# Performance work log

Measured on AMD Instinct MI355X. Metric: run time of the kernel, lower is better.

Reference implementation:

```python
import jax, jax.numpy as jnp
import numpy as np

K = 8            # NEAREST_K
IN = 68          # input_size = 64 + 4
EO = 32          # edge_output_size
FEAT = IN * 2 + EO * 4  # 264
EMB = 32         # linear_embedding
NCLS = 2
N = 768
EPS = 1e-5


def lrelu(x):
    return jnp.where(x >= 0, x, 0.01 * x)


def setup_inputs() -> dict:
    key = jax.random.key(0)
    ks = jax.random.split(key, 16)

    def w(k, fan_in, fan_out):
        return jax.random.normal(k, (fan_in, fan_out), jnp.float32) / np.float32(np.sqrt(fan_in))

    return {
        "feat0": jax.random.normal(ks[0], (N, IN), jnp.float32),
        "feat1": jax.random.normal(ks[1], (N, IN), jnp.float32),
        # edge_conv1: Linear(IN*K, EO) -> LeakyReLU -> Linear(EO, EO) -> LeakyReLU
        "ec1_w1": w(ks[2], IN * K, EO), "ec1_b1": jnp.zeros((EO,), jnp.float32),
        "ec1_w2": w(ks[3], EO, EO),     "ec1_b2": jnp.zeros((EO,), jnp.float32),
        # edge_conv2: Linear(EO*K, EO) -> LeakyReLU -> Linear(EO, EO) -> LeakyReLU
        "ec2_w1": w(ks[4], EO * K, EO), "ec2_b1": jnp.zeros((EO,), jnp.float32),
        "ec2_w2": w(ks[5], EO, EO),     "ec2_b2": jnp.zeros((EO,), jnp.float32),
        # linear head: BN(FEAT) -> Linear(FEAT,EMB) -> LReLU -> Linear(EMB,EMB) -> LReLU -> Linear(EMB,NCLS)
        "bn_g": jnp.ones((FEAT,), jnp.float32), "bn_b": jnp.zeros((FEAT,), jnp.float32),
        "lin1_w": w(ks[6], FEAT, EMB), "lin1_b": jnp.zeros((EMB,), jnp.float32),
        "lin2_w": w(ks[7], EMB, EMB),  "lin2_b": jnp.zeros((EMB,), jnp.float32),
        "lin3_w": w(ks[8], EMB, NCLS), "lin3_b": jnp.zeros((NCLS,), jnp.float32),
    }


def _pairs_for_graph(feat, ec1_w1, ec1_b1, ec1_w2, ec1_b2,
                     ec2_w1, ec2_b1, ec2_w2, ec2_b2):
    n = feat.shape[0]
    # kNN on first 4 dims via pairwise L1 distance (includes self, dist 0)
    coords = feat[:, :4]
    dist = jnp.abs(coords[:, None, :] - coords[None, :, :]).sum(-1)  # [n, n]
    _, idx = jax.lax.top_k(-dist, K)  # [n, K] smallest distances

    # EdgeConv 1: gather neighbor features, flatten feature-major (matches torch transpose+view)
    e1 = feat[idx]                                  # [n, K, IN]
    e1 = jnp.swapaxes(e1, 1, 2).reshape(n, IN * K)  # [n, IN*K]
    e1 = lrelu(lrelu(e1 @ ec1_w1 + ec1_b1) @ ec1_w2 + ec1_b2)  # [n, EO]

    # EdgeConv 2 on edge1 outputs
    e2 = e1[idx]                                    # [n, K, EO]
    e2 = jnp.swapaxes(e2, 1, 2).reshape(n, EO * K)  # [n, EO*K]
    e2 = lrelu(lrelu(e2 @ ec2_w1 + ec2_b1) @ ec2_w2 + ec2_b2)  # [n, EO]

    x = jnp.concatenate([feat, e1, e2], axis=-1)    # [n, IN + 2*EO] = [n, 132]
    # upper-triangle (i<j) all-pairs concat, row-major order == torch masked_select of triu mask
    iu, ju = jnp.triu_indices(n, k=1)
    return jnp.concatenate([x[iu], x[ju]], axis=-1)  # [n(n-1)/2, FEAT]


def reference(feat0, feat1, ec1_w1, ec1_b1, ec1_w2, ec1_b2,
              ec2_w1, ec2_b1, ec2_w2, ec2_b2,
              bn_g, bn_b, lin1_w, lin1_b, lin2_w, lin2_b, lin3_w, lin3_b):
    ec = (ec1_w1, ec1_b1, ec1_w2, ec1_b2, ec2_w1, ec2_b1, ec2_w2, ec2_b2)
    x = jnp.concatenate([_pairs_for_graph(feat0, *ec),
                         _pairs_for_graph(feat1, *ec)], axis=0)  # [P, FEAT]
    # BatchNorm1d in training mode: batch statistics (biased variance)
    mu = x.mean(axis=0)
    var = x.var(axis=0)
    x = (x - mu) * jax.lax.rsqrt(var + EPS) * bn_g + bn_b
    x = lrelu(x @ lin1_w + lin1_b)
    x = lrelu(x @ lin2_w + lin2_b)
    return x @ lin3_w + lin3_b  # [P, NCLS]
```

## Files before the change

### kernel.cpp

```cpp
#include <hip/hip_runtime.h>

#define NN 768
#define IN_F 68
#define KNN 8
#define EO 32
#define FEAT 264
#define HALF_FEAT 132
#define EMB 32
#define NPAIR 294528

typedef __attribute__((ext_vector_type(8))) short bf16x8;
typedef __attribute__((ext_vector_type(4))) float f32x4;

static __device__ __forceinline__ int pack_chop2(float x0, float x1) {
  return __builtin_amdgcn_perm(__float_as_uint(x1), __float_as_uint(x0), 0x07060302);
}
static __device__ __forceinline__ float chop(float x) {
  return __uint_as_float(__float_as_uint(x) & 0xffff0000u);
}


__global__ void __launch_bounds__(128) topk_ec1_kernel(
    const float* __restrict__ feat0, const float* __restrict__ feat1,
    const float* __restrict__ w1, const float* __restrict__ b1,
    const float* __restrict__ w2, const float* __restrict__ b2,
    int* __restrict__ idx_out, float* __restrict__ e1out)
{
  const int i = blockIdx.x, g = blockIdx.y;
  const float* __restrict__ feat = g ? feat1 : feat0;
  const int tid = threadIdx.x;
  const int lane = tid & 63, wv = tid >> 6;

  __shared__ unsigned long long keys[128*8];
  __shared__ int nbr[8];
  __shared__ float gl[KNN*IN_F];
  __shared__ float hsh[EO];
  __shared__ float part1[2][EO];
  __shared__ float part2[4][EO];

  const float4 ci = *(const float4*)(feat + i*IN_F);

  float4 cand[6];
#pragma unroll
  for (int t = 0; t < 6; t++)
    cand[t] = *(const float4*)(feat + (tid + 128*t)*IN_F);

  float bd[8]; int bidx[8];
#pragma unroll
  for (int k = 0; k < 8; k++) { bd[k] = 1e30f; bidx[k] = 0; }
#pragma unroll
  for (int t = 0; t < 6; t++) {
    const int j = tid + 128*t;
    float d = fabsf(ci.x - cand[t].x);
    d += fabsf(ci.y - cand[t].y);
    d += fabsf(ci.z - cand[t].z);
    d += fabsf(ci.w - cand[t].w);
    if (d < bd[7]) {
#pragma unroll
      for (int k = 7; k >= 1; k--) {
        if (d < bd[k-1])    { bd[k] = bd[k-1]; bidx[k] = bidx[k-1]; }
        else if (d < bd[k]) { bd[k] = d;       bidx[k] = j; }
      }
      if (d < bd[0]) { bd[0] = d; bidx[0] = j; }
    }
  }
#pragma unroll
  for (int k = 0; k < 8; k++)
    keys[tid*8+k] = ((unsigned long long)__float_as_uint(bd[k]) << 32) | (unsigned)bidx[k];
  __syncthreads();

  if (wv == 0) {
    int posA = 0, posB = 0;
#pragma unroll
    for (int r = 0; r < 8; r++) {
      unsigned long long ha = keys[lane*8 + posA];
      unsigned long long hb = keys[(lane+64)*8 + posB];
      unsigned long long mn = ha < hb ? ha : hb;
#pragma unroll
      for (int s = 32; s >= 1; s >>= 1) {
        unsigned long long o = __shfl_xor(mn, s, 64);
        mn = (o < mn) ? o : mn;
      }
      if (ha == mn) posA++;
      else if (hb == mn) posB++;
      if (lane == 0) {
        int nb = (int)(mn & 0xffffffffull);
        nbr[r] = nb;
        idx_out[(g*NN+i)*8 + r] = nb;
      }
    }
  }
  __syncthreads();

  for (int z = tid; z < KNN*17; z += 128) {
    int k = z / 17, q = z - k*17;
    *(float4*)&gl[k*IN_F + q*4] = *(const float4*)(feat + nbr[k]*IN_F + q*4);
  }
  __syncthreads();

  const int e = lane & 31, hf = lane >> 5;
  float ak[4];
#pragma unroll
  for (int k = 0; k < 4; k++) ak[k] = 0.f;
  const int cbeg = hf*34;
  const int kbase = wv*4;
  for (int c = cbeg; c < cbeg+34; c++) {
#pragma unroll
    for (int k = 0; k < 4; k++)
      ak[k] += gl[(kbase+k)*IN_F+c] * w1[(c*8+kbase+k)*EO + e];
  }
  float acc = (ak[0]+ak[1])+(ak[2]+ak[3]);
  acc += __shfl_xor(acc, 32, 64);
  if (hf == 0) part1[wv][e] = acc;
  __syncthreads();
  if (tid < 32) {
    float h = part1[0][tid] + part1[1][tid] + b1[tid];
    hsh[tid] = fmaxf(h, 0.01f*h);
  }
  __syncthreads();

  const int qq = tid >> 5, ee = tid & 31;
  {
    float o0=0.f, o1=0.f, o2=0.f, o3=0.f;
    const int mbeg = qq*8;
#pragma unroll
    for (int m = mbeg; m < mbeg+8; m += 4) {
      o0 += hsh[m+0] * w2[(m+0)*EO + ee];
      o1 += hsh[m+1] * w2[(m+1)*EO + ee];
      o2 += hsh[m+2] * w2[(m+2)*EO + ee];
      o3 += hsh[m+3] * w2[(m+3)*EO + ee];
    }
    part2[qq][ee] = ((o0+o1)+(o2+o3));
  }
  __syncthreads();
  if (tid < 32) {
    float o = b2[tid] + ((part2[0][tid]+part2[1][tid])+(part2[2][tid]+part2[3][tid]));
    o = fmaxf(o, 0.01f*o);
    e1out[(g*NN+i)*EO + tid] = o;
  }
}

__global__ void __launch_bounds__(64) ec2_kernel(
    const int* __restrict__ idx, const float* __restrict__ e1,
    const float* __restrict__ w1, const float* __restrict__ b1,
    const float* __restrict__ w2, const float* __restrict__ b2,
    float* __restrict__ e2out)
{
  const int i = blockIdx.x, g = blockIdx.y;
  const int lane = threadIdx.x;
  __shared__ float gl[KNN*EO];
  __shared__ float hsh[EO];
  {
    const int k = lane >> 3, q = lane & 7;
    const int nb = idx[(g*NN+i)*8 + k];
    *(float4*)&gl[k*EO + q*4] = *(const float4*)(e1 + (g*NN+nb)*EO + q*4);
  }
  __syncthreads();
  const int e = lane & 31, hf = lane >> 5;
  float ak[8];
#pragma unroll
  for (int k = 0; k < 8; k++) ak[k] = 0.f;
  const int cbeg = hf*16;
  for (int c = cbeg; c < cbeg+16; c++) {
#pragma unroll
    for (int k = 0; k < 8; k++)
      ak[k] += gl[k*EO+c] * w1[(c*8+k)*EO + e];
  }
  float acc = ((ak[0]+ak[1])+(ak[2]+ak[3])) + ((ak[4]+ak[5])+(ak[6]+ak[7]));
  acc += __shfl_xor(acc, 32, 64);
  if (hf == 0) {
    float h = acc + b1[e];
    hsh[e] = fmaxf(h, 0.01f*h);
  }
  __syncthreads();
  if (lane < 32) {
    float o0=0.f, o1=0.f, o2=0.f, o3=0.f;
#pragma unroll
    for (int m = 0; m < 32; m += 4) {
      o0 += hsh[m+0] * w2[(m+0)*EO + lane];
      o1 += hsh[m+1] * w2[(m+1)*EO + lane];
      o2 += hsh[m+2] * w2[(m+2)*EO + lane];
      o3 += hsh[m+3] * w2[(m+3)*EO + lane];
    }
    float o = b2[lane] + ((o0+o1)+(o2+o3));
    o = fmaxf(o, 0.01f*o);
    e2out[(g*NN+i)*EO + lane] = o;
  }
}

__global__ void __launch_bounds__(256) stats_kernel(
    const float* __restrict__ feat0, const float* __restrict__ feat1,
    const float* __restrict__ e1, const float* __restrict__ e2,
    const float* __restrict__ bn_g,
    float* __restrict__ mu_out, float* __restrict__ sg_out)
{
  const int c = blockIdx.x;
  const int tid = threadIdx.x;
  double s1=0, s2=0, q1=0, q2=0;
  for (int t = tid; t < 2*NN; t += 256) {
    int g = t >= NN;
    int i = t - g*NN;
    float val;
    if (c < IN_F)      val = (g ? feat1 : feat0)[i*IN_F + c];
    else if (c < 100)  val = e1[(g*NN+i)*EO + (c-IN_F)];
    else               val = e2[(g*NN+i)*EO + (c-100)];
    double dv = val;
    double wf = (double)(NN-1-i), wsnd = (double)i;
    s1 += wf*dv;  s2 += wsnd*dv;
    double dq = dv*dv;
    q1 += wf*dq;  q2 += wsnd*dq;
  }
#pragma unroll
  for (int off = 32; off >= 1; off >>= 1) {
    s1 += __shfl_xor(s1, off, 64);
    s2 += __shfl_xor(s2, off, 64);
    q1 += __shfl_xor(q1, off, 64);
    q2 += __shfl_xor(q2, off, 64);
  }
  __shared__ double red[4][4];
  const int w = tid >> 6;
  if ((tid & 63) == 0) { red[w][0]=s1; red[w][1]=s2; red[w][2]=q1; red[w][3]=q2; }
  __syncthreads();
  if (tid == 0) {
    double t0 = red[0][0]+red[1][0]+red[2][0]+red[3][0];
    double t1 = red[0][1]+red[1][1]+red[2][1]+red[3][1];
    double t2 = red[0][2]+red[1][2]+red[2][2]+red[3][2];
    double t3 = red[0][3]+red[1][3]+red[2][3]+red[3][3];
    const double M2 = 2.0 * (double)NPAIR;
    double mu1 = t0/M2, mu2 = t1/M2;
    double v1 = t2/M2 - mu1*mu1;
    double v2 = t3/M2 - mu2*mu2;
    mu_out[c]           = (float)mu1;
    mu_out[HALF_FEAT+c] = (float)mu2;
    sg_out[c]           = (float)((double)bn_g[c] / sqrt(v1 + 1e-5));
    sg_out[HALF_FEAT+c] = (float)((double)bn_g[HALF_FEAT+c] / sqrt(v2 + 1e-5));
  }
}

__global__ void __launch_bounds__(64) uv_c0_kernel(
    const float* __restrict__ feat0, const float* __restrict__ feat1,
    const float* __restrict__ e1, const float* __restrict__ e2,
    const float* __restrict__ sg, const float* __restrict__ mu,
    const float* __restrict__ bn_b,
    const float* __restrict__ lin1_w, const float* __restrict__ lin1_b,
    float* __restrict__ u, float* __restrict__ v, float* __restrict__ c0g)
{
  const int i = blockIdx.x, g = blockIdx.y;
  const int t = threadIdx.x;
  if (i == NN) {
    if (g == 0 && t < EMB) {
      float a0=0.f, a1=0.f, a2=0.f, a3=0.f;
      for (int c = 0; c < FEAT; c += 4) {
        a0 += (bn_b[c+0] - mu[c+0]*sg[c+0]) * lin1_w[(c+0)*EMB + t];
        a1 += (bn_b[c+1] - mu[c+1]*sg[c+1]) * lin1_w[(c+1)*EMB + t];
        a2 += (bn_b[c+2] - mu[c+2]*sg[c+2]) * lin1_w[(c+2)*EMB + t];
        a3 += (bn_b[c+3] - mu[c+3]*sg[c+3]) * lin1_w[(c+3)*EMB + t];
      }
      c0g[t] = lin1_b[t] + ((a0+a1)+(a2+a3));
    }
    return;
  }
  __shared__ float x[HALF_FEAT];
  for (int c = t; c < IN_F; c += 64) x[c] = (g ? feat1 : feat0)[i*IN_F + c];
  if (t < 32) x[IN_F + t]     = e1[(g*NN+i)*EO + t];
  else        x[100 + (t-32)] = e2[(g*NN+i)*EO + (t-32)];
  __syncthreads();
  const int e = t & 31, hf = t >> 5;
  const int base = hf * HALF_FEAT;
  float a0=0.f, a1=0.f, a2=0.f, a3=0.f;
  for (int c = 0; c < HALF_FEAT; c += 4) {
    a0 += x[c+0] * sg[base+c+0] * lin1_w[(base+c+0)*EMB + e];
    a1 += x[c+1] * sg[base+c+1] * lin1_w[(base+c+1)*EMB + e];
    a2 += x[c+2] * sg[base+c+2] * lin1_w[(base+c+2)*EMB + e];
    a3 += x[c+3] * sg[base+c+3] * lin1_w[(base+c+3)*EMB + e];
  }
  float acc = ((a0+a1)+(a2+a3));
  float* dst = hf ? v : u;
  dst[(g*NN+i)*EMB + e] = acc;
}

__global__ void __launch_bounds__(256) pair_kernel(
    const float* __restrict__ u, const float* __restrict__ v,
    const float* __restrict__ c0g,
    const float* __restrict__ lin2_w, const float* __restrict__ lin2_b,
    const float* __restrict__ lin3_w, const float* __restrict__ lin3_b,
    float2* __restrict__ out)
{
  const int g = blockIdx.y;
  int rem = blockIdx.x;
  int a = 0;
  while (rem >= 48 - a) { rem -= 48 - a; a++; }
  const int b = a + rem;

  __shared__ float su[16*36], sv[16*36];
  __shared__ float wbuf[4][16*36];
  const int tid = threadIdx.x;
  {
    int r = tid >> 5, c = tid & 31;
    su[r*36+c] = u[(g*NN + a*16 + r)*EMB + c];
    sv[r*36+c] = v[(g*NN + b*16 + r)*EMB + c];
    r += 8;
    su[r*36+c] = u[(g*NN + a*16 + r)*EMB + c];
    sv[r*36+c] = v[(g*NN + b*16 + r)*EMB + c];
  }
  __syncthreads();

  const int lane = tid & 63, w = tid >> 6;
  const int q = lane & 15, kg = lane >> 4;

  union { int i[4]; bf16x8 v; } whi0, wlo0, whi1, wlo1;
#pragma unroll
  for (int d = 0; d < 4; d++) {
    float w0a = lin2_w[(kg*8+2*d)*32 + q];
    float w0b = lin2_w[(kg*8+2*d+1)*32 + q];
    float w1a = lin2_w[(kg*8+2*d)*32 + 16 + q];
    float w1b = lin2_w[(kg*8+2*d+1)*32 + 16 + q];
    whi0.i[d] = pack_chop2(w0a, w0b);
    wlo0.i[d] = pack_chop2(w0a - chop(w0a), w0b - chop(w0b));
    whi1.i[d] = pack_chop2(w1a, w1b);
    wlo1.i[d] = pack_chop2(w1a - chop(w1a), w1b - chop(w1b));
  }
  float svc[8];
#pragma unroll
  for (int jj = 0; jj < 8; jj++)
    svc[jj] = sv[q*36 + kg*8 + jj] + c0g[kg*8+jj];
  float2 w3v[8]; float b2v[8];
#pragma unroll
  for (int jj = 0; jj < 8; jj++) {
    w3v[jj] = ((const float2*)lin3_w)[kg*8+jj];
    b2v[jj] = lin2_b[kg*8+jj];
  }
  const float b30 = lin3_b[0], b31 = lin3_b[1];

  float* wb = wbuf[w];
#pragma unroll
  for (int t = 0; t < 4; t++) {
    const int ty = w*4 + t;
    const float4 sa = *(const float4*)&su[ty*36 + kg*8];
    const float4 sb = *(const float4*)&su[ty*36 + kg*8 + 4];
    float se[8] = {sa.x, sa.y, sa.z, sa.w, sb.x, sb.y, sb.z, sb.w};
    union { int i[4]; bf16x8 v; } ahi, alo;
#pragma unroll
    for (int d = 0; d < 4; d++) {
      float s0 = se[2*d]   + svc[2*d];
      float s1 = se[2*d+1] + svc[2*d+1];
      s0 = fmaxf(s0, 0.01f*s0);
      s1 = fmaxf(s1, 0.01f*s1);
      ahi.i[d] = pack_chop2(s0, s1);
      alo.i[d] = pack_chop2(s0 - chop(s0), s1 - chop(s1));
    }
    f32x4 acc0 = {0.f,0.f,0.f,0.f}, acc1 = {0.f,0.f,0.f,0.f};
    acc0 = __builtin_amdgcn_mfma_f32_16x16x32_bf16(ahi.v, whi0.v, acc0, 0,0,0);
    acc1 = __builtin_amdgcn_mfma_f32_16x16x32_bf16(ahi.v, whi1.v, acc1, 0,0,0);
    acc0 = __builtin_amdgcn_mfma_f32_16x16x32_bf16(ahi.v, wlo0.v, acc0, 0,0,0);
    acc1 = __builtin_amdgcn_mfma_f32_16x16x32_bf16(ahi.v, wlo1.v, acc1, 0,0,0);
    acc0 = __builtin_amdgcn_mfma_f32_16x16x32_bf16(alo.v, whi0.v, acc0, 0,0,0);
    acc1 = __builtin_amdgcn_mfma_f32_16x16x32_bf16(alo.v, whi1.v, acc1, 0,0,0);
#pragma unroll
    for (int r = 0; r < 4; r++) {
      wb[(kg*4+r)*36 + q]      = acc0[r];
      wb[(kg*4+r)*36 + 16 + q] = acc1[r];
    }
    float o0 = 0.f, o1 = 0.f;
#pragma unroll
    for (int jj = 0; jj < 8; jj++) {
      float h = wb[q*36 + kg*8 + jj] + b2v[jj];
      h = fmaxf(h, 0.01f*h);
      o0 += h * w3v[jj].x;
      o1 += h * w3v[jj].y;
    }
    o0 += __shfl_xor(o0, 16, 64); o0 += __shfl_xor(o0, 32, 64);
    o1 += __shfl_xor(o1, 16, 64); o1 += __shfl_xor(o1, 32, 64);
    const int i = a*16 + ty, j = b*16 + q;
    if (lane < 16 && j > i) {
      long p = (long)i*NN - (long)i*(i+1)/2 + (j - i - 1);
      out[(long)g*NPAIR + p] = make_float2(o0 + b30, o1 + b31);
    }
  }
}

extern "C" void kernel_launch(void* const* d_in, const int* in_sizes, int n_in,
                              void* d_out, int out_size, void* d_ws, size_t ws_size,
                              hipStream_t stream)
{
  const float* feat0  = (const float*)d_in[0];
  const float* feat1  = (const float*)d_in[1];
  const float* ec1_w1 = (const float*)d_in[2];
  const float* ec1_b1 = (const float*)d_in[3];
  const float* ec1_w2 = (const float*)d_in[4];
  const float* ec1_b2 = (const float*)d_in[5];
  const float* ec2_w1 = (const float*)d_in[6];
  const float* ec2_b1 = (const float*)d_in[7];
  const float* ec2_w2 = (const float*)d_in[8];
  const float* ec2_b2 = (const float*)d_in[9];
  const float* bn_g   = (const float*)d_in[10];
  const float* bn_b   = (const float*)d_in[11];
  const float* lin1_w = (const float*)d_in[12];
  const float* lin1_b = (const float*)d_in[13];
  const float* lin2_w = (const float*)d_in[14];
  const float* lin2_b = (const float*)d_in[15];
  const float* lin3_w = (const float*)d_in[16];
  const float* lin3_b = (const float*)d_in[17];

  char* ws = (char*)d_ws;
  int*   idx = (int*)  (ws + 0);
  float* e1  = (float*)(ws + 49152);
  float* e2  = (float*)(ws + 245760);
  float* u   = (float*)(ws + 442368);
  float* v   = (float*)(ws + 638976);
  float* mu  = (float*)(ws + 835584);
  float* sg  = (float*)(ws + 836640);
  float* c0g = (float*)(ws + 837696);

  topk_ec1_kernel<<<dim3(768,2), 128, 0, stream>>>(feat0, feat1, ec1_w1, ec1_b1,
                                                   ec1_w2, ec1_b2, idx, e1);
  ec2_kernel<<<dim3(768,2), 64, 0, stream>>>(idx, e1, ec2_w1, ec2_b1,
                                             ec2_w2, ec2_b2, e2);
  stats_kernel<<<dim3(132), 256, 0, stream>>>(feat0, feat1, e1, e2, bn_g, mu, sg);
  uv_c0_kernel<<<dim3(769,2), 64, 0, stream>>>(feat0, feat1, e1, e2, sg, mu, bn_b,
                                               lin1_w, lin1_b, u, v, c0g);
  pair_kernel<<<dim3(1176,2), 256, 0, stream>>>(u, v, c0g, lin2_w, lin2_b,
                                                lin3_w, lin3_b, (float2*)d_out);
}
```

Baseline: 134.4 us.

## Fuse lin1 projection and bias precompute into pair kernel

Removes the separate uv_c0 kernel and has each pair block compute its own u/v projections for its two 16-row tiles, plus the BN-folded bias c0, directly from features, e1/e2 and lin1_w. This drops one launch and the global round-trip for u, v and c0. In exchange each of the 2352 blocks redundantly does a 132x32 projection for 32 rows and a 264x32 bias reduction. It also reuses the feature staging buffer as the per-wave scratch space.

New measurement: 155.1 us. 1.15x slower.

```diff
diff --git a/kernel.cpp b/kernel.cpp
--- a/kernel.cpp
+++ b/kernel.cpp
@@ -237,71 +237,87 @@
   }
 }
 
-__global__ void __launch_bounds__(64) uv_c0_kernel(
+__global__ void __launch_bounds__(256) pair_kernel(
     const float* __restrict__ feat0, const float* __restrict__ feat1,
     const float* __restrict__ e1, const float* __restrict__ e2,
     const float* __restrict__ sg, const float* __restrict__ mu,
     const float* __restrict__ bn_b,
     const float* __restrict__ lin1_w, const float* __restrict__ lin1_b,
-    float* __restrict__ u, float* __restrict__ v, float* __restrict__ c0g)
-{
-  const int i = blockIdx.x, g = blockIdx.y;
-  const int t = threadIdx.x;
-  if (i == NN) {
-    if (g == 0 && t < EMB) {
-      float a0=0.f, a1=0.f, a2=0.f, a3=0.f;
-      for (int c = 0; c < FEAT; c += 4) {
-        a0 += (bn_b[c+0] - mu[c+0]*sg[c+0]) * lin1_w[(c+0)*EMB + t];
-        a1 += (bn_b[c+1] - mu[c+1]*sg[c+1]) * lin1_w[(c+1)*EMB + t];
-        a2 += (bn_b[c+2] - mu[c+2]*sg[c+2]) * lin1_w[(c+2)*EMB + t];
-        a3 += (bn_b[c+3] - mu[c+3]*sg[c+3]) * lin1_w[(c+3)*EMB + t];
-      }
-      c0g[t] = lin1_b[t] + ((a0+a1)+(a2+a3));
-    }
-    return;
-  }
-  __shared__ float x[HALF_FEAT];
-  for (int c = t; c < IN_F; c += 64) x[c] = (g ? feat1 : feat0)[i*IN_F + c];
-  if (t < 32) x[IN_F + t]     = e1[(g*NN+i)*EO + t];
-  else        x[100 + (t-32)] = e2[(g*NN+i)*EO + (t-32)];
-  __syncthreads();
-  const int e = t & 31, hf = t >> 5;
-  const int base = hf * HALF_FEAT;
-  float a0=0.f, a1=0.f, a2=0.f, a3=0.f;
-  for (int c = 0; c < HALF_FEAT; c += 4) {
-    a0 += x[c+0] * sg[base+c+0] * lin1_w[(base+c+0)*EMB + e];
-    a1 += x[c+1] * sg[base+c+1] * lin1_w[(base+c+1)*EMB + e];
-    a2 += x[c+2] * sg[base+c+2] * lin1_w[(base+c+2)*EMB + e];
-    a3 += x[c+3] * sg[base+c+3] * lin1_w[(base+c+3)*EMB + e];
-  }
-  float acc = ((a0+a1)+(a2+a3));
-  float* dst = hf ? v : u;
-  dst[(g*NN+i)*EMB + e] = acc;
-}
-
-__global__ void __launch_bounds__(256) pair_kernel(
-    const float* __restrict__ u, const float* __restrict__ v,
-    const float* __restrict__ c0g,
     const float* __restrict__ lin2_w, const float* __restrict__ lin2_b,
     const float* __restrict__ lin3_w, const float* __restrict__ lin3_b,
     float2* __restrict__ out)
 {
   const int g = blockIdx.y;
+  const float* __restrict__ feat = g ? feat1 : feat0;
   int rem = blockIdx.x;
   int a = 0;
   while (rem >= 48 - a) { rem -= 48 - a; a++; }
   const int b = a + rem;
 
+  __shared__ float xab[2][16][136];
   __shared__ float su[16*36], sv[16*36];
-  __shared__ float wbuf[4][16*36];
+  __shared__ float c0p[8][EMB];
+  __shared__ float c0s[EMB];
+
   const int tid = threadIdx.x;
+
   {
-    int r = tid >> 5, c = tid & 31;
-    su[r*36+c] = u[(g*NN + a*16 + r)*EMB + c];
-    sv[r*36+c] = v[(g*NN + b*16 + r)*EMB + c];
-    r += 8;
-    su[r*36+c] = u[(g*NN + a*16 + r)*EMB + c];
-    sv[r*36+c] = v[(g*NN + b*16 + r)*EMB + c];
+    const int r = tid >> 4, q = tid & 15;
+    const int ia = a*16 + r, ib = b*16 + r;
+    for (int c = q; c < HALF_FEAT; c += 16) {
+      float va, vb;
+      if (c < IN_F)      { va = feat[ia*IN_F + c];            vb = feat[ib*IN_F + c]; }
+      else if (c < 100)  { va = e1[(g*NN+ia)*EO + (c-IN_F)];  vb = e1[(g*NN+ib)*EO + (c-IN_F)]; }
+      else               { va = e2[(g*NN+ia)*EO + (c-100)];   vb = e2[(g*NN+ib)*EO + (c-100)]; }
+      xab[0][r][c] = va * sg[c];
+      xab[1][r][c] = vb * sg[HALF_FEAT + c];
+    }
+  }
+  {
+    const int e = tid & 31, grp = tid >> 5;
+    float p0=0.f, p1=0.f, p2=0.f;
+    const int cb = grp*33;
+    for (int c = cb; c < cb+33; c += 3) {
+      p0 += (bn_b[c+0] - mu[c+0]*sg[c+0]) * lin1_w[(c+0)*EMB + e];
+      p1 += (bn_b[c+1] - mu[c+1]*sg[c+1]) * lin1_w[(c+1)*EMB + e];
+      p2 += (bn_b[c+2] - mu[c+2]*sg[c+2]) * lin1_w[(c+2)*EMB + e];
+    }
+    c0p[grp][e] = (p0+p1)+p2;
+  }
+  __syncthreads();
+
+  {
+    const int e = tid & 31, rr = tid >> 5;
+    float u0a=0.f,u0b=0.f,u0c=0.f,u0d=0.f, u1a=0.f,u1b=0.f,u1c=0.f,u1d=0.f;
+    float v0a=0.f,v0b=0.f,v0c=0.f,v0d=0.f, v1a=0.f,v1b=0.f,v1c=0.f,v1d=0.f;
+    for (int c = 0; c < HALF_FEAT; c += 4) {
+      const float w0 = lin1_w[(c+0)*EMB + e];
+      const float w1_ = lin1_w[(c+1)*EMB + e];
+      const float w2_ = lin1_w[(c+2)*EMB + e];
+      const float w3_ = lin1_w[(c+3)*EMB + e];
+      const float z0 = lin1_w[(HALF_FEAT+c+0)*EMB + e];
+      const float z1 = lin1_w[(HALF_FEAT+c+1)*EMB + e];
+      const float z2 = lin1_w[(HALF_FEAT+c+2)*EMB + e];
+      const float z3 = lin1_w[(HALF_FEAT+c+3)*EMB + e];
+      const float4 xa0 = *(const float4*)&xab[0][rr][c];
+      const float4 xa1 = *(const float4*)&xab[0][rr+8][c];
+      const float4 xb0 = *(const float4*)&xab[1][rr][c];
+      const float4 xb1 = *(const float4*)&xab[1][rr+8][c];
+      u0a += xa0.x*w0; u0b += xa0.y*w1_; u0c += xa0.z*w2_; u0d += xa0.w*w3_;
+      u1a += xa1.x*w0; u1b += xa1.y*w1_; u1c += xa1.z*w2_; u1d += xa1.w*w3_;
+      v0a += xb0.x*z0; v0b += xb0.y*z1;  v0c += xb0.z*z2;  v0d += xb0.w*z3;
+      v1a += xb1.x*z0; v1b += xb1.y*z1;  v1c += xb1.z*z2;  v1d += xb1.w*z3;
+    }
+    su[rr*36 + e]     = (u0a+u0b)+(u0c+u0d);
+    su[(rr+8)*36 + e] = (u1a+u1b)+(u1c+u1d);
+    sv[rr*36 + e]     = (v0a+v0b)+(v0c+v0d);
+    sv[(rr+8)*36 + e] = (v1a+v1b)+(v1c+v1d);
+  }
+  if (tid < EMB) {
+    float s = 0.f;
+#pragma unroll
+    for (int gq = 0; gq < 8; gq++) s += c0p[gq][tid];
+    c0s[tid] = lin1_b[tid] + s;
   }
   __syncthreads();
 
@@ -323,7 +339,7 @@
   float svc[8];
 #pragma unroll
   for (int jj = 0; jj < 8; jj++)
-    svc[jj] = sv[q*36 + kg*8 + jj] + c0g[kg*8+jj];
+    svc[jj] = sv[q*36 + kg*8 + jj] + c0s[kg*8+jj];
   float2 w3v[8]; float b2v[8];
 #pragma unroll
   for (int jj = 0; jj < 8; jj++) {
@@ -332,7 +348,7 @@
   }
   const float b30 = lin3_b[0], b31 = lin3_b[1];
 
-  float* wb = wbuf[w];
+  float* wb = ((float*)xab) + w*576;
 #pragma unroll
   for (int t = 0; t < 4; t++) {
     const int ty = w*4 + t;
@@ -406,19 +422,15 @@
   int*   idx = (int*)  (ws + 0);
   float* e1  = (float*)(ws + 49152);
   float* e2  = (float*)(ws + 245760);
-  float* u   = (float*)(ws + 442368);
-  float* v   = (float*)(ws + 638976);
   float* mu  = (float*)(ws + 835584);
   float* sg  = (float*)(ws + 836640);
-  float* c0g = (float*)(ws + 837696);
 
   topk_ec1_kernel<<<dim3(768,2), 128, 0, stream>>>(feat0, feat1, ec1_w1, ec1_b1,
                                                    ec1_w2, ec1_b2, idx, e1);
   ec2_kernel<<<dim3(768,2), 64, 0, stream>>>(idx, e1, ec2_w1, ec2_b1,
                                              ec2_w2, ec2_b2, e2);
   stats_kernel<<<dim3(132), 256, 0, stream>>>(feat0, feat1, e1, e2, bn_g, mu, sg);
-  uv_c0_kernel<<<dim3(769,2), 64, 0, stream>>>(feat0, feat1, e1, e2, sg, mu, bn_b,
-                                               lin1_w, lin1_b, u, v, c0g);
-  pair_kernel<<<dim3(1176,2), 256, 0, stream>>>(u, v, c0g, lin2_w, lin2_b,
+  pair_kernel<<<dim3(1176,2), 256, 0, stream>>>(feat0, feat1, e1, e2, sg, mu, bn_b,
+                                                lin1_w, lin1_b, lin2_w, lin2_b,
                                                 lin3_w, lin3_b, (float2*)d_out);
 }
```
